# Performance work log

Measured on AMD Instinct MI355X. Metric: run time of the kernel, lower is better.

The kernel has to match this reference:

```python
import jax, jax.numpy as jnp
import numpy as np

S = 4096
D_MODEL = 1024
D_INTERNAL = 4096


def setup_inputs() -> dict:
    key = jax.random.key(0)
    ks = jax.random.split(key, 12)
    s = 0.02
    return {
        "x": jax.random.normal(ks[0], (S, D_MODEL), dtype=jnp.float32),
        # projection weights stored as [d_in, d_out] so y = x @ W + b
        "Wq": jax.random.normal(ks[1], (D_MODEL, D_MODEL), dtype=jnp.float32) * s,
        "bq": jnp.zeros((D_MODEL,), dtype=jnp.float32),
        "Wk": jax.random.normal(ks[2], (D_MODEL, D_MODEL), dtype=jnp.float32) * s,
        "bk": jnp.zeros((D_MODEL,), dtype=jnp.float32),
        "Wv": jax.random.normal(ks[3], (D_MODEL, D_MODEL), dtype=jnp.float32) * s,
        "bv": jnp.zeros((D_MODEL,), dtype=jnp.float32),
        "W1": jax.random.normal(ks[4], (D_MODEL, D_INTERNAL), dtype=jnp.float32) * s,
        "b1": jnp.zeros((D_INTERNAL,), dtype=jnp.float32),
        "W2": jax.random.normal(ks[5], (D_INTERNAL, D_MODEL), dtype=jnp.float32) * s,
        "b2": jnp.zeros((D_MODEL,), dtype=jnp.float32),
    }


def reference(x, Wq, bq, Wk, bk, Wv, bv, W1, b1, W2, b2):
    # x: [S, D] (module is unbatched: k.transpose(0,1) implies 2-D input)
    d_model = x.shape[-1]
    q = x @ Wq + bq                         # [S, D]
    k = x @ Wk + bk                         # [S, D]
    v = x @ Wv + bv                         # [S, D]
    scores = (q @ k.T) / jnp.sqrt(jnp.asarray(d_model, x.dtype))  # [S, S]
    s = x.shape[0]
    causal = jnp.triu(jnp.ones((s, s), dtype=bool), k=1)           # True above diag
    scores = jnp.where(causal, jnp.asarray(-1e9, x.dtype), scores)
    attn = jax.nn.softmax(scores, axis=-1)  # [S, S]
    attended = attn @ v                     # [S, D]
    h = x + attended                        # residual 1
    ff = jax.nn.relu(h @ W1 + b1) @ W2 + b2 # 2-layer MLP
    out = h + ff                            # residual 2
    return (out, attn)
```

## Files before the change

kernel.cpp:

```cpp
#include <hip/hip_runtime.h>
#include <hip/hip_bf16.h>


typedef __attribute__((ext_vector_type(4))) float  f32x4;
typedef __attribute__((ext_vector_type(8))) short  bf16x8;
typedef __attribute__((ext_vector_type(4))) unsigned short us4;
typedef __attribute__((ext_vector_type(8))) unsigned short us8;

#define DEVINL __device__ __forceinline__

static constexpr int S   = 4096;
static constexpr int DM  = 1024;
static constexpr int DI  = 4096;

DEVINL unsigned short f2bf(float f) {
  union { float f; unsigned u; } v; v.f = f;
  unsigned r = v.u + 0x7fffu + ((v.u >> 16) & 1u);
  return (unsigned short)(r >> 16);
}

DEVINL void gld_lds16(const unsigned short* g, unsigned short* l) {
  __builtin_amdgcn_global_load_lds(
      (const __attribute__((address_space(1))) void*)g,
      (__attribute__((address_space(3))) void*)l,
      16, 0, 0);
}

__global__ void cvt_f32_bf16(const float* __restrict__ in,
                             unsigned short* __restrict__ out, long n) {
  long i = ((long)blockIdx.x * 256 + threadIdx.x) * 8;
  if (i >= n) return;
  f32x4 a = *(const f32x4*)(in + i);
  f32x4 b = *(const f32x4*)(in + i + 4);
  us8 o;
  o[0] = f2bf(a[0]); o[1] = f2bf(a[1]); o[2] = f2bf(a[2]); o[3] = f2bf(a[3]);
  o[4] = f2bf(b[0]); o[5] = f2bf(b[1]); o[6] = f2bf(b[2]); o[7] = f2bf(b[3]);
  *(us8*)(out + i) = o;
}

__global__ void transpose_cvt(const float* __restrict__ in,
                              unsigned short* __restrict__ out, int R, int C) {
  __shared__ float tile[32][33];
  const int bx = blockIdx.x * 32, by = blockIdx.y * 32;
  const int tx = threadIdx.x, ty = threadIdx.y;
  #pragma unroll
  for (int j = 0; j < 4; ++j) {
    int r = ty + j * 8;
    tile[r][tx] = in[(size_t)(by + r) * C + bx + tx];
  }
  __syncthreads();
  #pragma unroll
  for (int j = 0; j < 4; ++j) {
    int r = ty + j * 8;
    out[(size_t)(bx + r) * R + by + tx] = f2bf(tile[tx][r]);
  }
}

__global__ void transpose_bf16(const unsigned short* __restrict__ in, int ld,
                               unsigned short* __restrict__ out, int ldo) {
  __shared__ unsigned short tile[32][33];
  const int bx = blockIdx.x * 32, by = blockIdx.y * 32;
  const int tx = threadIdx.x, ty = threadIdx.y;
  #pragma unroll
  for (int j = 0; j < 4; ++j) {
    int r = ty + j * 8;
    tile[r][tx] = in[(size_t)(by + r) * ld + bx + tx];
  }
  __syncthreads();
  #pragma unroll
  for (int j = 0; j < 4; ++j) {
    int r = ty + j * 8;
    out[(size_t)(bx + r) * ldo + by + tx] = tile[tx][r];
  }
}

enum { EPI_QKV = 0, EPI_SC = 2, EPI_FF1 = 4, EPI_PART = 6 };

#define VM_WAIT4 asm volatile("s_waitcnt vmcnt(4)" ::: "memory")
#define VM_WAIT0 asm volatile("s_waitcnt vmcnt(0)" ::: "memory")

template <int EPI, bool TRI_PACK, bool TRI_TRUNC>
__launch_bounds__(512, 2)
__global__ void gemm8(const unsigned short* __restrict__ A,
                      const unsigned short* __restrict__ Bt,
                      int M, int N, int K, int lda, int ldb, int kChunk,
                      const float* __restrict__ bias,
                      float* __restrict__ Cf,
                      unsigned short* __restrict__ Cb,
                      float scale) {
  int bm, bn;
  if (TRI_PACK) {
    int t = blockIdx.x;
    bm = (int)((sqrtf(8.f * (float)t + 1.f) - 1.f) * 0.5f);
    while ((bm + 1) * (bm + 2) / 2 <= t) ++bm;
    while (bm * (bm + 1) / 2 > t) --bm;
    bn = t - bm * (bm + 1) / 2;
  } else { bm = blockIdx.y; bn = blockIdx.x; }
  const int bm0 = bm * 256, bn0 = bn * 256;

  const int kbeg = blockIdx.z * kChunk;
  int kend = min(K, kbeg + kChunk);
  if (TRI_TRUNC) kend = min(kend, bm0 + 256);
  const int len = kend - kbeg;
  const int NT = (len > 0) ? (len >> 6) : 0;

  __shared__ __align__(16) unsigned short lds[2 * 4 * 8192];

  const int tid  = threadIdx.x;
  const int lane = tid & 63;
  const int w    = tid >> 6;
  const int wr   = w >> 2, wc = w & 3;
  const int fr   = lane & 15, fq = lane >> 4;

  f32x4 acc[8][4] = {};

  const int tq = tid >> 2;
  const int swcolE = ((tid & 3) * 8) ^ ((tq & 6) << 2);
  const unsigned short* gA = A  + (size_t)(bm0 + tq) * lda + kbeg + swcolE;
  const unsigned short* gB = Bt + (size_t)(bn0 + tq) * ldb + kbeg + swcolE;
  const size_t aH = (size_t)128 * lda, bH = (size_t)128 * ldb;

  auto dstp = [&](int buf, int part, int h) {
    return (unsigned short*)lds + buf * 32768 + part * 8192 + h * 4096 + w * 512;
  };
  auto stA = [&](int buf, int t_, int ks) {
    const size_t go = (size_t)t_ * 64 + ks * 32;
    gld_lds16(gA + go,      dstp(buf, ks ? 2 : 0, 0));
    gld_lds16(gA + aH + go, dstp(buf, ks ? 2 : 0, 1));
  };
  auto stB = [&](int buf, int t_, int ks) {
    const size_t go = (size_t)t_ * 64 + ks * 32;
    gld_lds16(gB + go,      dstp(buf, ks ? 3 : 1, 0));
    gld_lds16(gB + bH + go, dstp(buf, ks ? 3 : 1, 1));
  };

  const int frSw = (fq * 8) ^ ((fr & 6) << 2);
  auto rdA = [&](int buf, int mi, int ks) {
    return *(const bf16x8*)((const unsigned short*)lds + buf * 32768 +
                            (ks ? 2 : 0) * 8192 + (wr * 128 + mi * 16 + fr) * 32 + frSw);
  };
  auto rdB = [&](int buf, int ni, int ks) {
    return *(const bf16x8*)((const unsigned short*)lds + buf * 32768 +
                            (ks ? 3 : 1) * 8192 + (wc * 64 + ni * 16 + fr) * 32 + frSw);
  };

  if (NT > 0) {
    stA(0, 0, 0); stB(0, 0, 0); stA(0, 0, 1); stB(0, 0, 1);
    VM_WAIT4;
    __builtin_amdgcn_s_barrier();

    for (int t = 0; t < NT; ++t) {
      const int cur = t & 1, nxt = cur ^ 1;
      const bool pf = (t + 1 < NT);
      bf16x8 a[8], p, q;

      #pragma unroll
      for (int mi = 0; mi < 8; ++mi) a[mi] = rdA(cur, mi, 0);
      p = rdB(cur, 0, 0); q = rdB(cur, 1, 0);
      if (pf) stA(nxt, t + 1, 0);
      __builtin_amdgcn_s_barrier();
      __builtin_amdgcn_s_setprio(1);
      #pragma unroll
      for (int mi = 0; mi < 8; ++mi) {
        acc[mi][0] = __builtin_amdgcn_mfma_f32_16x16x32_bf16(a[mi], p, acc[mi][0], 0, 0, 0);
        acc[mi][1] = __builtin_amdgcn_mfma_f32_16x16x32_bf16(a[mi], q, acc[mi][1], 0, 0, 0);
      }
      __builtin_amdgcn_s_setprio(0);
      __builtin_amdgcn_s_barrier();

      p = rdB(cur, 2, 0); q = rdB(cur, 3, 0);
      if (pf) stB(nxt, t + 1, 0);
      __builtin_amdgcn_s_barrier();
      __builtin_amdgcn_s_setprio(1);
      #pragma unroll
      for (int mi = 0; mi < 8; ++mi) {
        acc[mi][2] = __builtin_amdgcn_mfma_f32_16x16x32_bf16(a[mi], p, acc[mi][2], 0, 0, 0);
        acc[mi][3] = __builtin_amdgcn_mfma_f32_16x16x32_bf16(a[mi], q, acc[mi][3], 0, 0, 0);
      }
      __builtin_amdgcn_s_setprio(0);
      if (pf) { VM_WAIT4; } else { VM_WAIT0; }
      __builtin_amdgcn_s_barrier();

      #pragma unroll
      for (int mi = 0; mi < 8; ++mi) a[mi] = rdA(cur, mi, 1);
      p = rdB(cur, 0, 1); q = rdB(cur, 1, 1);
      if (pf) stA(nxt, t + 1, 1);
      __builtin_amdgcn_s_barrier();
      __builtin_amdgcn_s_setprio(1);
      #pragma unroll
      for (int mi = 0; mi < 8; ++mi) {
        acc[mi][0] = __builtin_amdgcn_mfma_f32_16x16x32_bf16(a[mi], p, acc[mi][0], 0, 0, 0);
        acc[mi][1] = __builtin_amdgcn_mfma_f32_16x16x32_bf16(a[mi], q, acc[mi][1], 0, 0, 0);
      }
      __builtin_amdgcn_s_setprio(0);
      __builtin_amdgcn_s_barrier();

      p = rdB(cur, 2, 1); q = rdB(cur, 3, 1);
      if (pf) stB(nxt, t + 1, 1);
      __builtin_amdgcn_s_barrier();
      __builtin_amdgcn_s_setprio(1);
      #pragma unroll
      for (int mi = 0; mi < 8; ++mi) {
        acc[mi][2] = __builtin_amdgcn_mfma_f32_16x16x32_bf16(a[mi], p, acc[mi][2], 0, 0, 0);
        acc[mi][3] = __builtin_amdgcn_mfma_f32_16x16x32_bf16(a[mi], q, acc[mi][3], 0, 0, 0);
      }
      __builtin_amdgcn_s_setprio(0);
      if (pf) { VM_WAIT4; }
      __builtin_amdgcn_s_barrier();
    }
  }

  const int row0 = bm0 + wr * 128 + fq * 4;
  const int col0 = bn0 + wc * 64 + fr;
  const size_t zoff = (EPI == EPI_PART) ? (size_t)blockIdx.z * M * N : 0;
  #pragma unroll
  for (int ni = 0; ni < 4; ++ni) {
    const int col = col0 + ni * 16;
    float bval = 0.f;
    if (EPI == EPI_QKV || EPI == EPI_FF1) bval = bias[col];
    #pragma unroll
    for (int mi = 0; mi < 8; ++mi) {
      #pragma unroll
      for (int j = 0; j < 4; ++j) {
        const int row = row0 + mi * 16 + j;
        const size_t idx = zoff + (size_t)row * N + col;
        const float c = acc[mi][ni][j];
        if (EPI == EPI_QKV) {
          Cb[idx] = f2bf(c + bval);
        } else if (EPI == EPI_SC) {
          Cf[idx] = c * scale;
        } else if (EPI == EPI_FF1) {
          const float r = c + bval;
          Cb[idx] = f2bf(r > 0.f ? r : 0.f);
        } else {
          Cf[idx] = c;
        }
      }
    }
  }
}

template <bool FINAL, int Z>
__global__ void reduce_k(const float* __restrict__ P,
                         const float* __restrict__ res,
                         const float* __restrict__ bias,
                         float* __restrict__ outf,
                         unsigned short* __restrict__ outb, long n) {
  long i = ((long)blockIdx.x * 256 + threadIdx.x) * 4;
  if (i >= n) return;
  f32x4 a = *(const f32x4*)(P + i);
  #pragma unroll
  for (int z = 1; z < Z; ++z) {
    f32x4 b = *(const f32x4*)(P + (size_t)z * n + i);
    #pragma unroll
    for (int j = 0; j < 4; ++j) a[j] += b[j];
  }
  f32x4 r = *(const f32x4*)(res + i);
  if (FINAL) {
    f32x4 bb = *(const f32x4*)(bias + (i & (DM - 1)));
    f32x4 o;
    #pragma unroll
    for (int j = 0; j < 4; ++j) o[j] = a[j] + r[j] + bb[j];
    *(f32x4*)(outf + i) = o;
  } else {
    f32x4 o; us4 ob;
    #pragma unroll
    for (int j = 0; j < 4; ++j) { o[j] = a[j] + r[j]; ob[j] = f2bf(o[j]); }
    *(f32x4*)(outf + i) = o;
    *(us4*)(outb + i) = ob;
  }
}

__global__ void softmax_rows(float* __restrict__ sc,
                             unsigned short* __restrict__ attnb) {
  const int m = blockIdx.x;
  const int tid = threadIdx.x;
  const int valid = m + 1;
  float* rowf = sc + (size_t)m * S;
  unsigned short* rowb = attnb + (size_t)m * S;

  f32x4 v[4];
  float lmax = -1e30f;
  #pragma unroll
  for (int i = 0; i < 4; ++i) {
    if (i * 1024 <= m) {
      const int idx = tid * 4 + i * 1024;
      v[i] = *(const f32x4*)(rowf + idx);
      #pragma unroll
      for (int j = 0; j < 4; ++j)
        if (idx + j < valid) lmax = fmaxf(lmax, v[i][j]);
    }
  }
  #pragma unroll
  for (int off = 32; off > 0; off >>= 1)
    lmax = fmaxf(lmax, __shfl_xor(lmax, off, 64));

  __shared__ float red[8];
  if ((tid & 63) == 0) red[tid >> 6] = lmax;
  __syncthreads();
  lmax = fmaxf(fmaxf(red[0], red[1]), fmaxf(red[2], red[3]));

  f32x4 e[4];
  float lsum = 0.f;
  #pragma unroll
  for (int i = 0; i < 4; ++i) {
    const int idx = tid * 4 + i * 1024;
    #pragma unroll
    for (int j = 0; j < 4; ++j) e[i][j] = 0.f;
    if (i * 1024 <= m) {
      #pragma unroll
      for (int j = 0; j < 4; ++j) {
        const float ev = (idx + j < valid) ? __expf(v[i][j] - lmax) : 0.f;
        e[i][j] = ev;
        lsum += ev;
      }
    }
  }
  #pragma unroll
  for (int off = 32; off > 0; off >>= 1)
    lsum += __shfl_xor(lsum, off, 64);
  if ((tid & 63) == 0) red[4 + (tid >> 6)] = lsum;
  __syncthreads();
  const float tsum = red[4] + red[5] + red[6] + red[7];
  const float inv = 1.0f / tsum;

  #pragma unroll
  for (int i = 0; i < 4; ++i) {
    const int idx = tid * 4 + i * 1024;
    f32x4 o; us4 ob;
    #pragma unroll
    for (int j = 0; j < 4; ++j) {
      const float t = e[i][j] * inv;
      o[j] = t;
      ob[j] = f2bf(t);
    }
    *(f32x4*)(rowf + idx) = o;
    *(us4*)(rowb + idx) = ob;
  }
}

extern "C" void kernel_launch(void* const* d_in, const int* in_sizes, int n_in,
                              void* d_out, int out_size, void* d_ws, size_t ws_size,
                              hipStream_t stream) {
  const float* x  = (const float*)d_in[0];
  const float* Wq = (const float*)d_in[1];
  const float* bq = (const float*)d_in[2];
  const float* Wk = (const float*)d_in[3];
  const float* bk = (const float*)d_in[4];
  const float* Wv = (const float*)d_in[5];
  const float* bv = (const float*)d_in[6];
  const float* W1 = (const float*)d_in[7];
  const float* b1 = (const float*)d_in[8];
  const float* W2 = (const float*)d_in[9];
  const float* b2 = (const float*)d_in[10];
  (void)in_sizes; (void)n_in; (void)out_size;

  float* outp  = (float*)d_out;
  float* attnf = (float*)d_out + (size_t)S * DM;

  const size_t MB = 1ull << 20;
  char* ws = (char*)d_ws;
  unsigned short* W2t   = (unsigned short*)(ws + 0 * MB);
  unsigned short* W1t   = (unsigned short*)(ws + 8 * MB);
  float*          h     = (float*)(ws + 16 * MB);
  unsigned short* hb    = (unsigned short*)(ws + 32 * MB);
  unsigned short* vt    = (unsigned short*)(ws + 40 * MB);
  unsigned short* attnb = (unsigned short*)(ws + 48 * MB);
  unsigned short* qkv   = (unsigned short*)(ws + 80 * MB);
  unsigned short* xb    = (unsigned short*)(ws + 104 * MB);
  unsigned short* Wqkvt = (unsigned short*)(ws + 112 * MB);
  float*          bqkv  = (float*)(ws + 118 * MB);
  unsigned short* ff1b  = (unsigned short*)(ws + 40 * MB);
  float*          Ppv   = (float*)(ws + 80 * MB);
  float*          Pff   = (float*)(ws + 72 * MB);

  const bool big = ws_size >= 145 * MB;

  cvt_f32_bf16<<<dim3((S * DM) / 2048), 256, 0, stream>>>(x, xb, (long)S * DM);
  transpose_cvt<<<dim3(DM / 32, DM / 32), dim3(32, 8), 0, stream>>>(Wq, Wqkvt, DM, DM);
  transpose_cvt<<<dim3(DM / 32, DM / 32), dim3(32, 8), 0, stream>>>(Wk, Wqkvt + (size_t)DM * DM, DM, DM);
  transpose_cvt<<<dim3(DM / 32, DM / 32), dim3(32, 8), 0, stream>>>(Wv, Wqkvt + 2 * (size_t)DM * DM, DM, DM);
  transpose_cvt<<<dim3(DI / 32, DM / 32), dim3(32, 8), 0, stream>>>(W1, W1t, DM, DI);
  transpose_cvt<<<dim3(DM / 32, DI / 32), dim3(32, 8), 0, stream>>>(W2, W2t, DI, DM);
  hipMemcpyAsync(bqkv,          bq, DM * sizeof(float), hipMemcpyDeviceToDevice, stream);
  hipMemcpyAsync(bqkv + DM,     bk, DM * sizeof(float), hipMemcpyDeviceToDevice, stream);
  hipMemcpyAsync(bqkv + 2 * DM, bv, DM * sizeof(float), hipMemcpyDeviceToDevice, stream);

  gemm8<EPI_QKV, false, false><<<dim3(3072 / 256, S / 256, 1), 512, 0, stream>>>(
      xb, Wqkvt, S, 3072, DM, DM, DM, DM, bqkv, nullptr, qkv, 1.f);
  transpose_bf16<<<dim3(DM / 32, S / 32), dim3(32, 8), 0, stream>>>(
      qkv + 2 * DM, 3072, vt, S);

  gemm8<EPI_SC, true, false><<<dim3(136, 1, 1), 512, 0, stream>>>(
      qkv, qkv + DM, S, S, DM, 3072, 3072, DM, nullptr, attnf, nullptr, 0.03125f);

  softmax_rows<<<dim3(S), 256, 0, stream>>>(attnf, attnb);

  if (big) {
    gemm8<EPI_PART, false, true><<<dim3(DM / 256, S / 256, 4), 512, 0, stream>>>(
        attnb, vt, S, DM, S, S, S, S / 4, nullptr, Ppv, nullptr, 1.f);
    reduce_k<false, 4><<<dim3((S * DM) / 1024), 256, 0, stream>>>(
        Ppv, x, nullptr, h, hb, (long)S * DM);
  } else {
    gemm8<EPI_PART, false, true><<<dim3(DM / 256, S / 256, 2), 512, 0, stream>>>(
        attnb, vt, S, DM, S, S, S, S / 2, nullptr, Ppv, nullptr, 1.f);
    reduce_k<false, 2><<<dim3((S * DM) / 1024), 256, 0, stream>>>(
        Ppv, x, nullptr, h, hb, (long)S * DM);
  }

  gemm8<EPI_FF1, false, false><<<dim3(DI / 256, S / 256, 1), 512, 0, stream>>>(
      hb, W1t, S, DI, DM, DM, DM, DM, b1, nullptr, ff1b, 1.f);

  if (big) {
    gemm8<EPI_PART, false, false><<<dim3(DM / 256, S / 256, 4), 512, 0, stream>>>(
        ff1b, W2t, S, DM, DI, DI, DI, DI / 4, nullptr, Pff, nullptr, 1.f);
    reduce_k<true, 4><<<dim3((S * DM) / 1024), 256, 0, stream>>>(
        Pff, h, b2, outp, nullptr, (long)S * DM);
  } else {
    gemm8<EPI_PART, false, false><<<dim3(DM / 256, S / 256, 2), 512, 0, stream>>>(
        ff1b, W2t, S, DM, DI, DI, DI, DI / 2, nullptr, Pff, nullptr, 1.f);
    reduce_k<true, 2><<<dim3((S * DM) / 1024), 256, 0, stream>>>(
        Pff, h, b2, outp, nullptr, (long)S * DM);
  }
}
```

Before: 289.2 us.

## Replace fine-grained ping-pong GEMM mainloop with simple 32-wide K double buffer

The GEMM main loop drops the interleaved four-phase schedule, with its extra barriers, setprio hints and partial vmcnt waits over 64-wide K tiles. It now uses a plain double buffer over 32-wide K tiles, with one staged load and one full wait per iteration. LDS use is halved, which could allow more resident blocks. In exchange, the loop runs twice as many iterations, each ending in a full vmcnt(0) wait and a barrier, so less memory latency is hidden behind MFMA work.

```diff
diff --git a/kernel.cpp b/kernel.cpp
--- a/kernel.cpp
+++ b/kernel.cpp
@@ -76,7 +76,6 @@
 
 enum { EPI_QKV = 0, EPI_SC = 2, EPI_FF1 = 4, EPI_PART = 6 };
 
-#define VM_WAIT4 asm volatile("s_waitcnt vmcnt(4)" ::: "memory")
 #define VM_WAIT0 asm volatile("s_waitcnt vmcnt(0)" ::: "memory")
 
 template <int EPI, bool TRI_PACK, bool TRI_TRUNC>
@@ -102,9 +101,9 @@
   int kend = min(K, kbeg + kChunk);
   if (TRI_TRUNC) kend = min(kend, bm0 + 256);
   const int len = kend - kbeg;
-  const int NT = (len > 0) ? (len >> 6) : 0;
-
-  __shared__ __align__(16) unsigned short lds[2 * 4 * 8192];
+  const int NT = (len > 0) ? (len >> 5) : 0;
+
+  __shared__ __align__(16) unsigned short lds[2 * 16384];
 
   const int tid  = threadIdx.x;
   const int lane = tid & 63;
@@ -120,92 +119,48 @@
   const unsigned short* gB = Bt + (size_t)(bn0 + tq) * ldb + kbeg + swcolE;
   const size_t aH = (size_t)128 * lda, bH = (size_t)128 * ldb;
 
-  auto dstp = [&](int buf, int part, int h) {
-    return (unsigned short*)lds + buf * 32768 + part * 8192 + h * 4096 + w * 512;
+  auto stage = [&](int buf, int t_) {
+    unsigned short* base = (unsigned short*)lds + buf * 16384;
+    const size_t go = (size_t)t_ * 32;
+    gld_lds16(gA + go,      base + w * 512);
+    gld_lds16(gA + aH + go, base + 4096 + w * 512);
+    gld_lds16(gB + go,      base + 8192 + w * 512);
+    gld_lds16(gB + bH + go, base + 12288 + w * 512);
   };
-  auto stA = [&](int buf, int t_, int ks) {
-    const size_t go = (size_t)t_ * 64 + ks * 32;
-    gld_lds16(gA + go,      dstp(buf, ks ? 2 : 0, 0));
-    gld_lds16(gA + aH + go, dstp(buf, ks ? 2 : 0, 1));
+
+  const int frSw = (fq * 8) ^ ((fr & 6) << 2);
+  auto rdA = [&](int buf, int mi) {
+    return *(const bf16x8*)((const unsigned short*)lds + buf * 16384 +
+                            (wr * 128 + mi * 16 + fr) * 32 + frSw);
   };
-  auto stB = [&](int buf, int t_, int ks) {
-    const size_t go = (size_t)t_ * 64 + ks * 32;
-    gld_lds16(gB + go,      dstp(buf, ks ? 3 : 1, 0));
-    gld_lds16(gB + bH + go, dstp(buf, ks ? 3 : 1, 1));
+  auto rdB = [&](int buf, int ni) {
+    return *(const bf16x8*)((const unsigned short*)lds + buf * 16384 + 8192 +
+                            (wc * 64 + ni * 16 + fr) * 32 + frSw);
   };
 
-  const int frSw = (fq * 8) ^ ((fr & 6) << 2);
-  auto rdA = [&](int buf, int mi, int ks) {
-    return *(const bf16x8*)((const unsigned short*)lds + buf * 32768 +
-                            (ks ? 2 : 0) * 8192 + (wr * 128 + mi * 16 + fr) * 32 + frSw);
-  };
-  auto rdB = [&](int buf, int ni, int ks) {
-    return *(const bf16x8*)((const unsigned short*)lds + buf * 32768 +
-                            (ks ? 3 : 1) * 8192 + (wc * 64 + ni * 16 + fr) * 32 + frSw);
-  };
-
   if (NT > 0) {
-    stA(0, 0, 0); stB(0, 0, 0); stA(0, 0, 1); stB(0, 0, 1);
-    VM_WAIT4;
+    stage(0, 0);
+    VM_WAIT0;
     __builtin_amdgcn_s_barrier();
 
     for (int t = 0; t < NT; ++t) {
       const int cur = t & 1, nxt = cur ^ 1;
       const bool pf = (t + 1 < NT);
-      bf16x8 a[8], p, q;
-
-      #pragma unroll
-      for (int mi = 0; mi < 8; ++mi) a[mi] = rdA(cur, mi, 0);
-      p = rdB(cur, 0, 0); q = rdB(cur, 1, 0);
-      if (pf) stA(nxt, t + 1, 0);
-      __builtin_amdgcn_s_barrier();
-      __builtin_amdgcn_s_setprio(1);
-      #pragma unroll
-      for (int mi = 0; mi < 8; ++mi) {
-        acc[mi][0] = __builtin_amdgcn_mfma_f32_16x16x32_bf16(a[mi], p, acc[mi][0], 0, 0, 0);
-        acc[mi][1] = __builtin_amdgcn_mfma_f32_16x16x32_bf16(a[mi], q, acc[mi][1], 0, 0, 0);
-      }
-      __builtin_amdgcn_s_setprio(0);
-      __builtin_amdgcn_s_barrier();
-
-      p = rdB(cur, 2, 0); q = rdB(cur, 3, 0);
-      if (pf) stB(nxt, t + 1, 0);
-      __builtin_amdgcn_s_barrier();
-      __builtin_amdgcn_s_setprio(1);
-      #pragma unroll
-      for (int mi = 0; mi < 8; ++mi) {
-        acc[mi][2] = __builtin_amdgcn_mfma_f32_16x16x32_bf16(a[mi], p, acc[mi][2], 0, 0, 0);
-        acc[mi][3] = __builtin_amdgcn_mfma_f32_16x16x32_bf16(a[mi], q, acc[mi][3], 0, 0, 0);
-      }
-      __builtin_amdgcn_s_setprio(0);
-      if (pf) { VM_WAIT4; } else { VM_WAIT0; }
-      __builtin_amdgcn_s_barrier();
-
-      #pragma unroll
-      for (int mi = 0; mi < 8; ++mi) a[mi] = rdA(cur, mi, 1);
-      p = rdB(cur, 0, 1); q = rdB(cur, 1, 1);
-      if (pf) stA(nxt, t + 1, 1);
-      __builtin_amdgcn_s_barrier();
-      __builtin_amdgcn_s_setprio(1);
-      #pragma unroll
-      for (int mi = 0; mi < 8; ++mi) {
-        acc[mi][0] = __builtin_amdgcn_mfma_f32_16x16x32_bf16(a[mi], p, acc[mi][0], 0, 0, 0);
-        acc[mi][1] = __builtin_amdgcn_mfma_f32_16x16x32_bf16(a[mi], q, acc[mi][1], 0, 0, 0);
-      }
-      __builtin_amdgcn_s_setprio(0);
-      __builtin_amdgcn_s_barrier();
-
-      p = rdB(cur, 2, 1); q = rdB(cur, 3, 1);
-      if (pf) stB(nxt, t + 1, 1);
-      __builtin_amdgcn_s_barrier();
-      __builtin_amdgcn_s_setprio(1);
-      #pragma unroll
-      for (int mi = 0; mi < 8; ++mi) {
-        acc[mi][2] = __builtin_amdgcn_mfma_f32_16x16x32_bf16(a[mi], p, acc[mi][2], 0, 0, 0);
-        acc[mi][3] = __builtin_amdgcn_mfma_f32_16x16x32_bf16(a[mi], q, acc[mi][3], 0, 0, 0);
-      }
-      __builtin_amdgcn_s_setprio(0);
-      if (pf) { VM_WAIT4; }
+      if (pf) stage(nxt, t + 1);
+
+      bf16x8 a[8], b[4];
+      #pragma unroll
+      for (int mi = 0; mi < 8; ++mi) a[mi] = rdA(cur, mi);
+      #pragma unroll
+      for (int ni = 0; ni < 4; ++ni) b[ni] = rdB(cur, ni);
+      #pragma unroll
+      for (int mi = 0; mi < 8; ++mi)
+        #pragma unroll
+        for (int ni = 0; ni < 4; ++ni)
+          acc[mi][ni] = __builtin_amdgcn_mfma_f32_16x16x32_bf16(
+              a[mi], b[ni], acc[mi][ni], 0, 0, 0);
+
+      if (pf) { VM_WAIT0; }
       __builtin_amdgcn_s_barrier();
     }
   }
```

Result: slower. 309.2 us (+6.9%).
